# Kernel optimization log

Measured on AMD Instinct MI355X. Metric: run time of the kernel, lower is better.

## Reference

```python
import jax, jax.numpy as jnp
import numpy as np

POOL_RATIO = 0.5  # SAGPooling default ratio


def graph_conv(x, src, dst, Wr, Wn, b, num_nodes):
    # PyG GraphConv (aggr='add'): h_i = x_i Wr + (sum_{j->i} x_j) Wn + b
    agg = jax.ops.segment_sum(x[src], dst, num_segments=num_nodes)
    return x @ Wr + agg @ Wn + b


def setup_inputs() -> dict:
    key = jax.random.key(0)
    ks = jax.random.split(key, 12)
    B, M, DF = 64, 512, 128           # batch, max_num_obj, per-feature dim
    N = B * M                          # 32768 flat nodes
    E = 524288                         # avg degree 16
    D_IN, D_OUT, L, C = 256, 256, 3, 11
    s_in = 1.0 / np.sqrt(D_IN)
    f0 = jax.random.normal(ks[0], (B, M, DF), jnp.float32)
    f1 = jax.random.normal(ks[1], (B, M, DF), jnp.float32)
    collated_edge_index = jax.random.randint(ks[2], (2, E), 0, N, dtype=jnp.int32)
    Wr = jax.random.normal(ks[3], (L, D_IN, D_OUT), jnp.float32) * s_in
    Wn = jax.random.normal(ks[4], (L, D_IN, D_OUT), jnp.float32) * s_in
    b = jax.random.normal(ks[5], (L, D_OUT), jnp.float32) * 0.01
    Wpr = jax.random.normal(ks[6], (D_OUT, 1), jnp.float32) * s_in
    Wpn = jax.random.normal(ks[7], (D_OUT, 1), jnp.float32) * s_in
    bp = jax.random.normal(ks[8], (1,), jnp.float32) * 0.01
    Wc = jax.random.normal(ks[9], (D_OUT, C), jnp.float32) * s_in
    bc = jax.random.normal(ks[10], (C,), jnp.float32) * 0.01
    return {"f0": f0, "f1": f1, "collated_edge_index": collated_edge_index,
            "Wr": Wr, "Wn": Wn, "b": b, "Wpr": Wpr, "Wpn": Wpn, "bp": bp,
            "Wc": Wc, "bc": bc}


def reference(f0, f1, collated_edge_index, Wr, Wn, b, Wpr, Wpn, bp, Wc, bc):
    # concat node features then flatten batch: [B, M, 2*DF] -> [N, D_IN]
    x = jnp.concatenate([f0, f1], axis=2)
    x = x.reshape(-1, x.shape[-1])
    N = x.shape[0]
    src, dst = collated_edge_index[0], collated_edge_index[1]
    for i in range(Wr.shape[0]):  # stacked GNN blocks + ReLU
        x = jax.nn.relu(graph_conv(x, src, dst, Wr[i], Wn[i], b[i], N))
    # SAGPooling: GraphConv attention score; source's batch tensor is constant
    # so top-k runs over all N nodes as one segment (ratio 0.5)
    score = graph_conv(x, src, dst, Wpr, Wpn, bp, N)[:, 0]
    k = int(np.ceil(POOL_RATIO * N))
    top_scores, perm = jax.lax.top_k(score, k)
    xp = x[perm] * jnp.tanh(top_scores)[:, None]   # [k, D_OUT]
    xp = jax.nn.relu(xp)
    logits = xp @ Wc + bc                          # [k, 11]
    return logits
```

## Files before the change

### kernel.cpp

```cpp
#include <hip/hip_runtime.h>
#include <hip/hip_bf16.h>
#include <math.h>
#include <stdint.h>


__global__ __launch_bounds__(256) void concat_kernel(const float* __restrict__ f0,
                                                     const float* __restrict__ f1,
                                                     float* __restrict__ x,
                                                     int N) {
    int gid = blockIdx.x * blockDim.x + threadIdx.x;
    int total = N * 64;
    if (gid >= total) return;
    int n = gid >> 6;
    int q = gid & 63;
    float4 v;
    if (q < 32) v = *(const float4*)(f0 + (size_t)n * 128 + q * 4);
    else        v = *(const float4*)(f1 + (size_t)n * 128 + (q - 32) * 4);
    *(float4*)(x + (size_t)n * 256 + q * 4) = v;
}

__global__ __launch_bounds__(256) void count_kernel(const int* __restrict__ dst,
                                                    int* __restrict__ counts, int E) {
    int e = blockIdx.x * blockDim.x + threadIdx.x;
    if (e < E) atomicAdd(&counts[dst[e]], 1);
}

__global__ __launch_bounds__(1024) void scan_kernel(int* __restrict__ counts,
                                                    int* __restrict__ offs,
                                                    int N, int E) {
    __shared__ int s[1024];
    int t = threadIdx.x;
    int base = t * 32;
    int local[32];
    int sum = 0;
    #pragma unroll
    for (int j = 0; j < 32; ++j) { local[j] = counts[base + j]; sum += local[j]; }
    s[t] = sum;
    __syncthreads();
    for (int off = 1; off < 1024; off <<= 1) {
        int other = (t >= off) ? s[t - off] : 0;
        __syncthreads();
        s[t] += other;
        __syncthreads();
    }
    int run = s[t] - sum;
    #pragma unroll
    for (int j = 0; j < 32; ++j) {
        offs[base + j] = run;
        run += local[j];
        counts[base + j] = 0;
    }
    if (t == 1023) offs[N] = E;
}

__global__ __launch_bounds__(256) void fill_kernel(const int* __restrict__ dst,
                                                   const int* __restrict__ offs,
                                                   int* __restrict__ cursor,
                                                   int* __restrict__ csr, int E) {
    int e = blockIdx.x * blockDim.x + threadIdx.x;
    if (e >= E) return;
    int d = dst[e];
    int pos = offs[d] + atomicAdd(&cursor[d], 1);
    csr[pos] = e;
}

__global__ __launch_bounds__(256) void bsort_kernel(int* __restrict__ csr,
                                                    const int* __restrict__ offs,
                                                    const int* __restrict__ src,
                                                    int N) {
    int i = blockIdx.x * blockDim.x + threadIdx.x;
    if (i >= N) return;
    int beg = offs[i], end = offs[i + 1];
    for (int a = beg + 1; a < end; ++a) {
        int v = csr[a];
        int b = a - 1;
        while (b >= beg && csr[b] > v) { csr[b + 1] = csr[b]; --b; }
        csr[b + 1] = v;
    }
    for (int p = beg; p < end; ++p) csr[p] = src[csr[p]];
}

__global__ __launch_bounds__(256) void segsum_kernel(const float* __restrict__ X,
                                                     const int* __restrict__ csr,
                                                     const int* __restrict__ offs,
                                                     float* __restrict__ AGG, int N) {
    int w = threadIdx.x >> 6;
    int lane = threadIdx.x & 63;
    int n = blockIdx.x * 4 + w;
    if (n >= N) return;
    int beg = offs[n], end = offs[n + 1];
    float4 acc = make_float4(0.f, 0.f, 0.f, 0.f);
    for (int p = beg; p < end; ++p) {
        int s = csr[p];
        float4 v = *(const float4*)(X + (size_t)s * 256 + lane * 4);
        acc.x += v.x; acc.y += v.y; acc.z += v.z; acc.w += v.w;
    }
    *(float4*)(AGG + (size_t)n * 256 + lane * 4) = acc;
}

#define GBM 128
#define GBN 128
#define GBK 32

#define GEMM_LOAD_STAGE(kt)                                                          \
    {                                                                                \
        const int kb = (kt) * GBK;                                                   \
        const float* Asrc = (kb < 256) ? X : G;                                      \
        const float* Wsrc = (kb < 256) ? W1 : W2;                                    \
        const int kloc = kb & 255;                                                   \
        a_st0 = *(const float4*)(Asrc + (size_t)(rowBase + ar) * 256 + kloc + ak);   \
        a_st1 = *(const float4*)(Asrc + (size_t)(rowBase + ar + 64) * 256 + kloc + ak); \
        a_st2 = *(const float4*)(Asrc + (size_t)(rowBase + ar) * 256 + kloc + 16 + ak); \
        a_st3 = *(const float4*)(Asrc + (size_t)(rowBase + ar + 64) * 256 + kloc + 16 + ak); \
        w_st0 = *(const float4*)(Wsrc + (size_t)(kloc + wk) * 256 + colBase + wc);   \
        w_st1 = *(const float4*)(Wsrc + (size_t)(kloc + wk + 8) * 256 + colBase + wc); \
        w_st2 = *(const float4*)(Wsrc + (size_t)(kloc + wk + 16) * 256 + colBase + wc); \
        w_st3 = *(const float4*)(Wsrc + (size_t)(kloc + wk + 24) * 256 + colBase + wc); \
    }

__global__ __launch_bounds__(256) void gemm_two_kernel(const float* __restrict__ X,
                                                       const float* __restrict__ G,
                                                       const float* __restrict__ W1,
                                                       const float* __restrict__ W2,
                                                       const float* __restrict__ bias,
                                                       float* __restrict__ Y) {
    __shared__ float As[GBK][GBM + 4];
    __shared__ float Ws[GBK][GBN + 4];
    const int tid = threadIdx.x;
    const int tcol = tid & 15;
    const int trow = tid >> 4;
    const int rowBase = blockIdx.y * GBM;
    const int colBase = blockIdx.x * GBN;

    const int ar = tid >> 2;
    const int ak = (tid & 3) * 4;
    const int wk = tid >> 5;
    const int wc = (tid & 31) * 4;

    float4 a_st0, a_st1, a_st2, a_st3, w_st0, w_st1, w_st2, w_st3;

    float acc[4][4][4];
    #pragma unroll
    for (int q = 0; q < 4; ++q)
        #pragma unroll
        for (int i = 0; i < 4; ++i)
            #pragma unroll
            for (int j = 0; j < 4; ++j) acc[q][i][j] = 0.f;

    GEMM_LOAD_STAGE(0);

    for (int kt = 0; kt < 512 / GBK; ++kt) {
        __syncthreads();
        #pragma unroll
        for (int j = 0; j < 4; ++j) {
            As[ak + j][ar]           = ((const float*)&a_st0)[j];
            As[ak + j][ar + 64]      = ((const float*)&a_st1)[j];
            As[16 + ak + j][ar]      = ((const float*)&a_st2)[j];
            As[16 + ak + j][ar + 64] = ((const float*)&a_st3)[j];
        }
        *(float4*)&Ws[wk][wc]      = w_st0;
        *(float4*)&Ws[wk + 8][wc]  = w_st1;
        *(float4*)&Ws[wk + 16][wc] = w_st2;
        *(float4*)&Ws[wk + 24][wc] = w_st3;
        __syncthreads();
        if (kt < 512 / GBK - 1) GEMM_LOAD_STAGE(kt + 1);
        #pragma unroll
        for (int kk = 0; kk < GBK; ++kk) {
            float a0[4], a1[4], w0[4], w1[4];
            *(float4*)a0 = *(const float4*)&As[kk][trow * 4];
            *(float4*)a1 = *(const float4*)&As[kk][64 + trow * 4];
            *(float4*)w0 = *(const float4*)&Ws[kk][tcol * 4];
            *(float4*)w1 = *(const float4*)&Ws[kk][64 + tcol * 4];
            #pragma unroll
            for (int i = 0; i < 4; ++i)
                #pragma unroll
                for (int j = 0; j < 4; ++j) {
                    acc[0][i][j] = fmaf(a0[i], w0[j], acc[0][i][j]);
                    acc[1][i][j] = fmaf(a0[i], w1[j], acc[1][i][j]);
                    acc[2][i][j] = fmaf(a1[i], w0[j], acc[2][i][j]);
                    acc[3][i][j] = fmaf(a1[i], w1[j], acc[3][i][j]);
                }
        }
    }
    #pragma unroll
    for (int h = 0; h < 2; ++h) {
        #pragma unroll
        for (int i = 0; i < 4; ++i) {
            const int row = rowBase + h * 64 + trow * 4 + i;
            #pragma unroll
            for (int g = 0; g < 2; ++g) {
                const int colb = colBase + g * 64 + tcol * 4;
                float o[4];
                #pragma unroll
                for (int j = 0; j < 4; ++j)
                    o[j] = fmaxf(acc[h * 2 + g][i][j] + bias[colb + j], 0.f);
                *(float4*)(Y + (size_t)row * 256 + colb) = *(const float4*)&o[0];
            }
        }
    }
}

__global__ __launch_bounds__(256) void dot_kernel(const float* __restrict__ X3,
                                                  const float* __restrict__ Wpr,
                                                  const float* __restrict__ Wpn,
                                                  double* __restrict__ yr,
                                                  double* __restrict__ yn, int N) {
    int w = threadIdx.x >> 6;
    int lane = threadIdx.x & 63;
    int n = blockIdx.x * 4 + w;
    if (n >= N) return;
    float4 xv = *(const float4*)(X3 + (size_t)n * 256 + lane * 4);
    float4 wr = *(const float4*)(Wpr + lane * 4);
    float4 wn = *(const float4*)(Wpn + lane * 4);
    double dr = (double)xv.x * wr.x + (double)xv.y * wr.y +
                (double)xv.z * wr.z + (double)xv.w * wr.w;
    double dn = (double)xv.x * wn.x + (double)xv.y * wn.y +
                (double)xv.z * wn.z + (double)xv.w * wn.w;
    #pragma unroll
    for (int o = 32; o > 0; o >>= 1) {
        dr += __shfl_down(dr, o, 64);
        dn += __shfl_down(dn, o, 64);
    }
    if (lane == 0) { yr[n] = dr; yn[n] = dn; }
}

__global__ __launch_bounds__(256) void score_gather_kernel(
        const double* __restrict__ yr, const double* __restrict__ yn,
        const int* __restrict__ csr, const int* __restrict__ offs,
        const float* __restrict__ bp,
        double* __restrict__ sc, unsigned long long* __restrict__ keys, int N) {
    int n = blockIdx.x * blockDim.x + threadIdx.x;
    if (n >= N) return;
    double s = yr[n] + (double)bp[0];
    int beg = offs[n], end = offs[n + 1];
    for (int p = beg; p < end; ++p) s += yn[csr[p]];
    sc[n] = s;
    long long sb = __double_as_longlong(s);
    keys[n] = (sb < 0) ? ~(unsigned long long)sb
                       : ((unsigned long long)sb | 0x8000000000000000ULL);
}

#define RTI 1024
#define RTJ 512
__global__ __launch_bounds__(256) void rank_count_kernel(
        const unsigned long long* __restrict__ keys,
        int* __restrict__ rankcnt, int N) {
    __shared__ __align__(16) unsigned long long sk[RTJ];
    const int tid = threadIdx.x;
    const int ibase = blockIdx.y * RTI;
    const int jbase = blockIdx.x * RTJ;

    unsigned long long ki[4];
    #pragma unroll
    for (int r = 0; r < 4; ++r) ki[r] = keys[ibase + r * 256 + tid];
    for (int t = tid; t < RTJ; t += 256) sk[t] = keys[jbase + t];
    __syncthreads();

    int cnt[4] = {0, 0, 0, 0};
    if (jbase + RTJ <= ibase) {
        for (int u = 0; u < RTJ; u += 8) {
            ulonglong2 p0 = *(const ulonglong2*)&sk[u];
            ulonglong2 p1 = *(const ulonglong2*)&sk[u + 2];
            ulonglong2 p2 = *(const ulonglong2*)&sk[u + 4];
            ulonglong2 p3 = *(const ulonglong2*)&sk[u + 6];
            #pragma unroll
            for (int r = 0; r < 4; ++r) {
                cnt[r] += (int)(p0.x >= ki[r]) + (int)(p0.y >= ki[r])
                        + (int)(p1.x >= ki[r]) + (int)(p1.y >= ki[r])
                        + (int)(p2.x >= ki[r]) + (int)(p2.y >= ki[r])
                        + (int)(p3.x >= ki[r]) + (int)(p3.y >= ki[r]);
            }
        }
    } else if (jbase >= ibase + RTI) {
        for (int u = 0; u < RTJ; u += 8) {
            ulonglong2 p0 = *(const ulonglong2*)&sk[u];
            ulonglong2 p1 = *(const ulonglong2*)&sk[u + 2];
            ulonglong2 p2 = *(const ulonglong2*)&sk[u + 4];
            ulonglong2 p3 = *(const ulonglong2*)&sk[u + 6];
            #pragma unroll
            for (int r = 0; r < 4; ++r) {
                cnt[r] += (int)(p0.x > ki[r]) + (int)(p0.y > ki[r])
                        + (int)(p1.x > ki[r]) + (int)(p1.y > ki[r])
                        + (int)(p2.x > ki[r]) + (int)(p2.y > ki[r])
                        + (int)(p3.x > ki[r]) + (int)(p3.y > ki[r]);
            }
        }
    } else {
        int thr[4];
        #pragma unroll
        for (int r = 0; r < 4; ++r) thr[r] = ibase + r * 256 + tid - jbase;
        for (int u = 0; u < RTJ; ++u) {
            unsigned long long kj = sk[u];
            #pragma unroll
            for (int r = 0; r < 4; ++r)
                cnt[r] += (kj > ki[r]) || (kj == ki[r] && u < thr[r]);
        }
    }
    #pragma unroll
    for (int r = 0; r < 4; ++r)
        atomicAdd(&rankcnt[ibase + r * 256 + tid], cnt[r]);
}

__global__ __launch_bounds__(256) void rank_scatter_kernel(
        const int* __restrict__ rankcnt,
        const double* __restrict__ sc,
        int* __restrict__ perm,
        double* __restrict__ topd, int N, int K) {
    int i = blockIdx.x * blockDim.x + threadIdx.x;
    if (i >= N) return;
    int rank = rankcnt[i];
    if (rank < K) { perm[rank] = i; topd[rank] = sc[i]; }
}

__global__ __launch_bounds__(256) void out_kernel(const float* __restrict__ X3,
                                                  const int* __restrict__ perm,
                                                  const double* __restrict__ topd,
                                                  const float* __restrict__ Wc,
                                                  const float* __restrict__ bc,
                                                  float* __restrict__ out, int K) {
    int w = threadIdx.x >> 6;
    int lane = threadIdx.x & 63;
    int r = blockIdx.x * 4 + w;
    if (r >= K) return;
    int p = perm[r];
    double t = tanh(topd[r]);
    float4 xv = *(const float4*)(X3 + (size_t)p * 256 + lane * 4);
    double xp[4];
    xp[0] = (double)xv.x * t; xp[1] = (double)xv.y * t;
    xp[2] = (double)xv.z * t; xp[3] = (double)xv.w * t;
    #pragma unroll
    for (int j = 0; j < 4; ++j) xp[j] = xp[j] > 0.0 ? xp[j] : 0.0;
    double acc[11];
    #pragma unroll
    for (int c = 0; c < 11; ++c) acc[c] = 0.0;
    #pragma unroll
    for (int j = 0; j < 4; ++j) {
        const float* wrow = Wc + (size_t)(lane * 4 + j) * 11;
        #pragma unroll
        for (int c = 0; c < 11; ++c) acc[c] += xp[j] * (double)wrow[c];
    }
    #pragma unroll
    for (int c = 0; c < 11; ++c) {
        double v = acc[c];
        #pragma unroll
        for (int o = 32; o > 0; o >>= 1) v += __shfl_down(v, o, 64);
        if (lane == 0) out[(size_t)r * 11 + c] = (float)(v + (double)bc[c]);
    }
}

extern "C" void kernel_launch(void* const* d_in, const int* in_sizes, int n_in,
                              void* d_out, int out_size, void* d_ws, size_t ws_size,
                              hipStream_t stream) {
    const float* f0  = (const float*)d_in[0];
    const float* f1  = (const float*)d_in[1];
    const int*   ei  = (const int*)d_in[2];
    const float* Wr  = (const float*)d_in[3];
    const float* Wn  = (const float*)d_in[4];
    const float* b   = (const float*)d_in[5];
    const float* Wpr = (const float*)d_in[6];
    const float* Wpn = (const float*)d_in[7];
    const float* bp  = (const float*)d_in[8];
    const float* Wc  = (const float*)d_in[9];
    const float* bc  = (const float*)d_in[10];
    float* out = (float*)d_out;

    const int N = in_sizes[0] / 128;
    const int E = in_sizes[2] / 2;
    const int K = (N + 1) / 2;
    const int L = in_sizes[5] / 256;

    const int* src = ei;
    const int* dst = ei + E;

    char* p = (char*)d_ws;
    auto take = [&](size_t bytes) {
        char* r = p;
        p += (bytes + 255) & ~(size_t)255;
        return r;
    };
    float*  xA      = (float*)take((size_t)N * 256 * 4);
    float*  xB      = (float*)take((size_t)N * 256 * 4);
    float*  agg     = (float*)take((size_t)N * 256 * 4);
    int*    counts  = (int*)take((size_t)N * 4);
    int*    offs    = (int*)take((size_t)(N + 1) * 4);
    int*    csr     = (int*)take((size_t)E * 4);
    double* sc      = (double*)take((size_t)N * 8);
    unsigned long long* keys = (unsigned long long*)take((size_t)N * 8);
    int*    rankcnt = (int*)take((size_t)N * 4);
    double* topd    = (double*)take((size_t)K * 8);
    int*    perm    = (int*)take((size_t)K * 4);
    double* yrv     = (double*)take((size_t)N * 8);
    double* ynv     = (double*)take((size_t)N * 8);
    (void)ws_size;

    hipMemsetAsync(counts, 0, (size_t)N * 4, stream);
    hipMemsetAsync(rankcnt, 0, (size_t)N * 4, stream);

    concat_kernel<<<(N * 64 + 255) / 256, 256, 0, stream>>>(f0, f1, xA, N);
    count_kernel<<<(E + 255) / 256, 256, 0, stream>>>(dst, counts, E);
    scan_kernel<<<1, 1024, 0, stream>>>(counts, offs, N, E);
    fill_kernel<<<(E + 255) / 256, 256, 0, stream>>>(dst, offs, counts, csr, E);
    bsort_kernel<<<(N + 255) / 256, 256, 0, stream>>>(csr, offs, src, N);

    float* xcur = xA;
    float* xnext = xB;
    for (int i = 0; i < L; ++i) {
        segsum_kernel<<<N / 4, 256, 0, stream>>>(xcur, csr, offs, agg, N);
        gemm_two_kernel<<<dim3(256 / GBN, N / GBM), 256, 0, stream>>>(
            xcur, agg, Wr + (size_t)i * 65536, Wn + (size_t)i * 65536,
            b + (size_t)i * 256, xnext);
        float* tmp = xcur; xcur = xnext; xnext = tmp;
    }
    dot_kernel<<<N / 4, 256, 0, stream>>>(xcur, Wpr, Wpn, yrv, ynv, N);
    score_gather_kernel<<<N / 256, 256, 0, stream>>>(yrv, ynv, csr, offs, bp, sc, keys, N);
    rank_count_kernel<<<dim3(N / RTJ, N / RTI), 256, 0, stream>>>(keys, rankcnt, N);
    rank_scatter_kernel<<<(N + 255) / 256, 256, 0, stream>>>(rankcnt, sc, perm, topd, N, K);
    out_kernel<<<K / 4, 256, 0, stream>>>(xcur, perm, topd, Wc, bc, out, K);
}
```

Before: 813.5 us.

## Split two-operand GEMM into K-split partial products plus combine-ReLU pass

```diff
diff --git a/kernel.cpp b/kernel.cpp
--- a/kernel.cpp
+++ b/kernel.cpp
@@ -101,6 +101,122 @@
 #define GBM 128
 #define GBN 128
 #define GBK 32
+
+#define GSPLIT_LOAD(kt)                                                              \
+    {                                                                                \
+        const int kloc = (kt) * GBK;                                                 \
+        a_st0 = *(const float4*)(A + (size_t)(rowBase + ar) * 256 + kloc + ak);      \
+        a_st1 = *(const float4*)(A + (size_t)(rowBase + ar + 64) * 256 + kloc + ak); \
+        a_st2 = *(const float4*)(A + (size_t)(rowBase + ar) * 256 + kloc + 16 + ak); \
+        a_st3 = *(const float4*)(A + (size_t)(rowBase + ar + 64) * 256 + kloc + 16 + ak); \
+        w_st0 = *(const float4*)(W + (size_t)(kloc + wk) * 256 + colBase + wc);      \
+        w_st1 = *(const float4*)(W + (size_t)(kloc + wk + 8) * 256 + colBase + wc);  \
+        w_st2 = *(const float4*)(W + (size_t)(kloc + wk + 16) * 256 + colBase + wc); \
+        w_st3 = *(const float4*)(W + (size_t)(kloc + wk + 24) * 256 + colBase + wc); \
+    }
+
+__global__ __launch_bounds__(256, 4) void gemm_split_kernel(
+        const float* __restrict__ X, const float* __restrict__ G,
+        const float* __restrict__ W1, const float* __restrict__ W2,
+        const float* __restrict__ bias,
+        float* __restrict__ P1, float* __restrict__ P2) {
+    __shared__ float As[GBK][GBM + 4];
+    __shared__ float Ws[GBK][GBN + 4];
+    const int tid = threadIdx.x;
+    const int tcol = tid & 15;
+    const int trow = tid >> 4;
+    const int rowBase = blockIdx.y * GBM;
+    const int colBase = blockIdx.x * GBN;
+    const int z = blockIdx.z;
+    const float* __restrict__ A = z ? G : X;
+    const float* __restrict__ W = z ? W2 : W1;
+    float* __restrict__ P = z ? P2 : P1;
+
+    const int ar = tid >> 2;
+    const int ak = (tid & 3) * 4;
+    const int wk = tid >> 5;
+    const int wc = (tid & 31) * 4;
+
+    float4 a_st0, a_st1, a_st2, a_st3, w_st0, w_st1, w_st2, w_st3;
+
+    float acc[4][4][4];
+    #pragma unroll
+    for (int q = 0; q < 4; ++q)
+        #pragma unroll
+        for (int i = 0; i < 4; ++i)
+            #pragma unroll
+            for (int j = 0; j < 4; ++j) acc[q][i][j] = 0.f;
+
+    GSPLIT_LOAD(0);
+
+    for (int kt = 0; kt < 256 / GBK; ++kt) {
+        __syncthreads();
+        #pragma unroll
+        for (int j = 0; j < 4; ++j) {
+            As[ak + j][ar]           = ((const float*)&a_st0)[j];
+            As[ak + j][ar + 64]      = ((const float*)&a_st1)[j];
+            As[16 + ak + j][ar]      = ((const float*)&a_st2)[j];
+            As[16 + ak + j][ar + 64] = ((const float*)&a_st3)[j];
+        }
+        *(float4*)&Ws[wk][wc]      = w_st0;
+        *(float4*)&Ws[wk + 8][wc]  = w_st1;
+        *(float4*)&Ws[wk + 16][wc] = w_st2;
+        *(float4*)&Ws[wk + 24][wc] = w_st3;
+        __syncthreads();
+        if (kt < 256 / GBK - 1) GSPLIT_LOAD(kt + 1);
+        #pragma unroll
+        for (int kk = 0; kk < GBK; ++kk) {
+            float a0[4], a1[4], w0[4], w1[4];
+            *(float4*)a0 = *(const float4*)&As[kk][trow * 4];
+            *(float4*)a1 = *(const float4*)&As[kk][64 + trow * 4];
+            *(float4*)w0 = *(const float4*)&Ws[kk][tcol * 4];
+            *(float4*)w1 = *(const float4*)&Ws[kk][64 + tcol * 4];
+            #pragma unroll
+            for (int i = 0; i < 4; ++i)
+                #pragma unroll
+                for (int j = 0; j < 4; ++j) {
+                    acc[0][i][j] = fmaf(a0[i], w0[j], acc[0][i][j]);
+                    acc[1][i][j] = fmaf(a0[i], w1[j], acc[1][i][j]);
+                    acc[2][i][j] = fmaf(a1[i], w0[j], acc[2][i][j]);
+                    acc[3][i][j] = fmaf(a1[i], w1[j], acc[3][i][j]);
+                }
+        }
+    }
+    #pragma unroll
+    for (int h = 0; h < 2; ++h) {
+        #pragma unroll
+        for (int i = 0; i < 4; ++i) {
+            const int row = rowBase + h * 64 + trow * 4 + i;
+            #pragma unroll
+            for (int g = 0; g < 2; ++g) {
+                const int colb = colBase + g * 64 + tcol * 4;
+                float o[4];
+                #pragma unroll
+                for (int j = 0; j < 4; ++j) {
+                    float v = acc[h * 2 + g][i][j];
+                    if (z == 0) v += bias[colb + j];
+                    o[j] = v;
+                }
+                *(float4*)(P + (size_t)row * 256 + colb) = *(const float4*)&o[0];
+            }
+        }
+    }
+}
+
+__global__ __launch_bounds__(256) void combine_relu_kernel(
+        const float* __restrict__ P1, const float* __restrict__ P2,
+        float* __restrict__ Y, int total4) {
+    int gid = blockIdx.x * 256 + threadIdx.x;
+    if (gid >= total4) return;
+    float4 a = ((const float4*)P1)[gid];
+    float4 b = ((const float4*)P2)[gid];
+    float4 o;
+    o.x = fmaxf(a.x + b.x, 0.f);
+    o.y = fmaxf(a.y + b.y, 0.f);
+    o.z = fmaxf(a.z + b.z, 0.f);
+    o.w = fmaxf(a.w + b.w, 0.f);
+    ((float4*)Y)[gid] = o;
+}
 
 #define GEMM_LOAD_STAGE(kt)                                                          \
     {                                                                                \
@@ -391,7 +507,8 @@
     int*    perm    = (int*)take((size_t)K * 4);
     double* yrv     = (double*)take((size_t)N * 8);
     double* ynv     = (double*)take((size_t)N * 8);
-    (void)ws_size;
+    float*  P2buf   = (float*)take((size_t)N * 256 * 4);
+    const bool use_split = (size_t)(p - (char*)d_ws) <= ws_size;
 
     hipMemsetAsync(counts, 0, (size_t)N * 4, stream);
     hipMemsetAsync(rankcnt, 0, (size_t)N * 4, stream);
@@ -406,9 +523,17 @@
     float* xnext = xB;
     for (int i = 0; i < L; ++i) {
         segsum_kernel<<<N / 4, 256, 0, stream>>>(xcur, csr, offs, agg, N);
-        gemm_two_kernel<<<dim3(256 / GBN, N / GBM), 256, 0, stream>>>(
-            xcur, agg, Wr + (size_t)i * 65536, Wn + (size_t)i * 65536,
-            b + (size_t)i * 256, xnext);
+        if (use_split) {
+            gemm_split_kernel<<<dim3(256 / GBN, N / GBM, 2), 256, 0, stream>>>(
+                xcur, agg, Wr + (size_t)i * 65536, Wn + (size_t)i * 65536,
+                b + (size_t)i * 256, xnext, P2buf);
+            combine_relu_kernel<<<(N * 64 + 255) / 256, 256, 0, stream>>>(
+                xnext, P2buf, xnext, N * 64);
+        } else {
+            gemm_two_kernel<<<dim3(256 / GBN, N / GBM), 256, 0, stream>>>(
+                xcur, agg, Wr + (size_t)i * 65536, Wn + (size_t)i * 65536,
+                b + (size_t)i * 256, xnext);
+        }
         float* tmp = xcur; xcur = xnext; xnext = tmp;
     }
     dot_kernel<<<N / 4, 256, 0, stream>>>(xcur, Wpr, Wpn, yrv, ynv, N);
```

Result: slower. 1.335 ms (+64.1%).

## Split GEMM into two K-halves across grid z and add combine-ReLU kernel

Applied to the files above, without the earlier changes.

```diff
diff --git a/kernel.cpp b/kernel.cpp
--- a/kernel.cpp
+++ b/kernel.cpp
@@ -100,104 +100,119 @@
 
 #define GBM 128
 #define GBN 128
-#define GBK 32
-
-#define GEMM_LOAD_STAGE(kt)                                                          \
-    {                                                                                \
-        const int kb = (kt) * GBK;                                                   \
-        const float* Asrc = (kb < 256) ? X : G;                                      \
-        const float* Wsrc = (kb < 256) ? W1 : W2;                                    \
-        const int kloc = kb & 255;                                                   \
-        a_st0 = *(const float4*)(Asrc + (size_t)(rowBase + ar) * 256 + kloc + ak);   \
-        a_st1 = *(const float4*)(Asrc + (size_t)(rowBase + ar + 64) * 256 + kloc + ak); \
-        a_st2 = *(const float4*)(Asrc + (size_t)(rowBase + ar) * 256 + kloc + 16 + ak); \
-        a_st3 = *(const float4*)(Asrc + (size_t)(rowBase + ar + 64) * 256 + kloc + 16 + ak); \
-        w_st0 = *(const float4*)(Wsrc + (size_t)(kloc + wk) * 256 + colBase + wc);   \
-        w_st1 = *(const float4*)(Wsrc + (size_t)(kloc + wk + 8) * 256 + colBase + wc); \
-        w_st2 = *(const float4*)(Wsrc + (size_t)(kloc + wk + 16) * 256 + colBase + wc); \
-        w_st3 = *(const float4*)(Wsrc + (size_t)(kloc + wk + 24) * 256 + colBase + wc); \
-    }
-
-__global__ __launch_bounds__(256) void gemm_two_kernel(const float* __restrict__ X,
-                                                       const float* __restrict__ G,
-                                                       const float* __restrict__ W1,
-                                                       const float* __restrict__ W2,
-                                                       const float* __restrict__ bias,
-                                                       float* __restrict__ Y) {
+#define GBK 16
+
+#define GSPLIT_LOAD(kt)                                                          \
+    {                                                                             \
+        const int kloc = (kt) * GBK;                                              \
+        const float* Abase = A + (size_t)(rowBase + tid) * 256 + kloc;            \
+        a_st0 = *(const float4*)(Abase + 0);                                      \
+        a_st1 = *(const float4*)(Abase + 4);                                      \
+        a_st2 = *(const float4*)(Abase + 8);                                      \
+        a_st3 = *(const float4*)(Abase + 12);                                     \
+        const float* Wbase = W + (size_t)(kloc + wk) * 256 + colBase + wc;        \
+        w_st0 = *(const float4*)(Wbase + 0);                                      \
+        w_st1 = *(const float4*)(Wbase + 4);                                      \
+        w_st2 = *(const float4*)(Wbase + 8);                                      \
+        w_st3 = *(const float4*)(Wbase + 12);                                     \
+    }
+
+__global__ __launch_bounds__(128) void gemm_split_kernel(
+        const float* __restrict__ X, const float* __restrict__ G,
+        const float* __restrict__ W1, const float* __restrict__ W2,
+        const float* __restrict__ bias,
+        float* __restrict__ P1, float* __restrict__ P2) {
     __shared__ float As[GBK][GBM + 4];
     __shared__ float Ws[GBK][GBN + 4];
     const int tid = threadIdx.x;
+    const int trow = tid >> 4;
     const int tcol = tid & 15;
-    const int trow = tid >> 4;
     const int rowBase = blockIdx.y * GBM;
     const int colBase = blockIdx.x * GBN;
-
-    const int ar = tid >> 2;
-    const int ak = (tid & 3) * 4;
-    const int wk = tid >> 5;
-    const int wc = (tid & 31) * 4;
+    const int z = blockIdx.z;
+    const float* __restrict__ A = z ? G : X;
+    const float* __restrict__ W = z ? W2 : W1;
+    float* __restrict__ P = z ? P2 : P1;
+
+    const int wk = tid >> 3;
+    const int wc = (tid & 7) * 16;
 
     float4 a_st0, a_st1, a_st2, a_st3, w_st0, w_st1, w_st2, w_st3;
 
-    float acc[4][4][4];
-    #pragma unroll
-    for (int q = 0; q < 4; ++q)
-        #pragma unroll
-        for (int i = 0; i < 4; ++i)
-            #pragma unroll
-            for (int j = 0; j < 4; ++j) acc[q][i][j] = 0.f;
-
-    GEMM_LOAD_STAGE(0);
-
-    for (int kt = 0; kt < 512 / GBK; ++kt) {
+    float acc[2][16][4];
+    #pragma unroll
+    for (int h = 0; h < 2; ++h)
+        #pragma unroll
+        for (int i = 0; i < 16; ++i)
+            #pragma unroll
+            for (int j = 0; j < 4; ++j) acc[h][i][j] = 0.f;
+
+    GSPLIT_LOAD(0);
+
+    for (int kt = 0; kt < 256 / GBK; ++kt) {
         __syncthreads();
         #pragma unroll
         for (int j = 0; j < 4; ++j) {
-            As[ak + j][ar]           = ((const float*)&a_st0)[j];
-            As[ak + j][ar + 64]      = ((const float*)&a_st1)[j];
-            As[16 + ak + j][ar]      = ((const float*)&a_st2)[j];
-            As[16 + ak + j][ar + 64] = ((const float*)&a_st3)[j];
+            As[j][tid]      = ((const float*)&a_st0)[j];
+            As[4 + j][tid]  = ((const float*)&a_st1)[j];
+            As[8 + j][tid]  = ((const float*)&a_st2)[j];
+            As[12 + j][tid] = ((const float*)&a_st3)[j];
         }
         *(float4*)&Ws[wk][wc]      = w_st0;
-        *(float4*)&Ws[wk + 8][wc]  = w_st1;
-        *(float4*)&Ws[wk + 16][wc] = w_st2;
-        *(float4*)&Ws[wk + 24][wc] = w_st3;
+        *(float4*)&Ws[wk][wc + 4]  = w_st1;
+        *(float4*)&Ws[wk][wc + 8]  = w_st2;
+        *(float4*)&Ws[wk][wc + 12] = w_st3;
         __syncthreads();
-        if (kt < 512 / GBK - 1) GEMM_LOAD_STAGE(kt + 1);
+        if (kt < 256 / GBK - 1) GSPLIT_LOAD(kt + 1);
         #pragma unroll
         for (int kk = 0; kk < GBK; ++kk) {
-            float a0[4], a1[4], w0[4], w1[4];
-            *(float4*)a0 = *(const float4*)&As[kk][trow * 4];
-            *(float4*)a1 = *(const float4*)&As[kk][64 + trow * 4];
-            *(float4*)w0 = *(const float4*)&Ws[kk][tcol * 4];
-            *(float4*)w1 = *(const float4*)&Ws[kk][64 + tcol * 4];
-            #pragma unroll
-            for (int i = 0; i < 4; ++i)
+            float a[16], w[8];
+            *(float4*)&a[0]  = *(const float4*)&As[kk][trow * 16];
+            *(float4*)&a[4]  = *(const float4*)&As[kk][trow * 16 + 4];
+            *(float4*)&a[8]  = *(const float4*)&As[kk][trow * 16 + 8];
+            *(float4*)&a[12] = *(const float4*)&As[kk][trow * 16 + 12];
+            *(float4*)&w[0]  = *(const float4*)&Ws[kk][tcol * 4];
+            *(float4*)&w[4]  = *(const float4*)&Ws[kk][64 + tcol * 4];
+            #pragma unroll
+            for (int i = 0; i < 16; ++i)
                 #pragma unroll
                 for (int j = 0; j < 4; ++j) {
-                    acc[0][i][j] = fmaf(a0[i], w0[j], acc[0][i][j]);
-                    acc[1][i][j] = fmaf(a0[i], w1[j], acc[1][i][j]);
-                    acc[2][i][j] = fmaf(a1[i], w0[j], acc[2][i][j]);
-                    acc[3][i][j] = fmaf(a1[i], w1[j], acc[3][i][j]);
+                    acc[0][i][j] = fmaf(a[i], w[j],     acc[0][i][j]);
+                    acc[1][i][j] = fmaf(a[i], w[4 + j], acc[1][i][j]);
                 }
         }
     }
     #pragma unroll
-    for (int h = 0; h < 2; ++h) {
-        #pragma unroll
-        for (int i = 0; i < 4; ++i) {
-            const int row = rowBase + h * 64 + trow * 4 + i;
-            #pragma unroll
-            for (int g = 0; g < 2; ++g) {
-                const int colb = colBase + g * 64 + tcol * 4;
-                float o[4];
-                #pragma unroll
-                for (int j = 0; j < 4; ++j)
-                    o[j] = fmaxf(acc[h * 2 + g][i][j] + bias[colb + j], 0.f);
-                *(float4*)(Y + (size_t)row * 256 + colb) = *(const float4*)&o[0];
+    for (int i = 0; i < 16; ++i) {
+        const int row = rowBase + trow * 16 + i;
+        #pragma unroll
+        for (int h = 0; h < 2; ++h) {
+            const int colb = colBase + h * 64 + tcol * 4;
+            float o[4];
+            #pragma unroll
+            for (int j = 0; j < 4; ++j) {
+                float v = acc[h][i][j];
+                if (z == 0) v += bias[colb + j];
+                o[j] = v;
             }
-        }
-    }
+            *(float4*)(P + (size_t)row * 256 + colb) = *(const float4*)&o[0];
+        }
+    }
+}
+
+__global__ __launch_bounds__(256) void combine_relu_kernel(
+        const float* __restrict__ P1, const float* __restrict__ P2,
+        float* __restrict__ Y, int total4) {
+    int gid = blockIdx.x * 256 + threadIdx.x;
+    if (gid >= total4) return;
+    float4 a = ((const float4*)P1)[gid];
+    float4 b = ((const float4*)P2)[gid];
+    float4 o;
+    o.x = fmaxf(a.x + b.x, 0.f);
+    o.y = fmaxf(a.y + b.y, 0.f);
+    o.z = fmaxf(a.z + b.z, 0.f);
+    o.w = fmaxf(a.w + b.w, 0.f);
+    ((float4*)Y)[gid] = o;
 }
 
 __global__ __launch_bounds__(256) void dot_kernel(const float* __restrict__ X3,
@@ -391,6 +406,7 @@
     int*    perm    = (int*)take((size_t)K * 4);
     double* yrv     = (double*)take((size_t)N * 8);
     double* ynv     = (double*)take((size_t)N * 8);
+    float*  P2buf   = (float*)take((size_t)N * 256 * 4);
     (void)ws_size;
 
     hipMemsetAsync(counts, 0, (size_t)N * 4, stream);
@@ -406,9 +422,11 @@
     float* xnext = xB;
     for (int i = 0; i < L; ++i) {
         segsum_kernel<<<N / 4, 256, 0, stream>>>(xcur, csr, offs, agg, N);
-        gemm_two_kernel<<<dim3(256 / GBN, N / GBM), 256, 0, stream>>>(
+        gemm_split_kernel<<<dim3(256 / GBN, N / GBM, 2), 128, 0, stream>>>(
             xcur, agg, Wr + (size_t)i * 65536, Wn + (size_t)i * 65536,
-            b + (size_t)i * 256, xnext);
+            b + (size_t)i * 256, xnext, P2buf);
+        combine_relu_kernel<<<(N * 64 + 255) / 256, 256, 0, stream>>>(
+            xnext, P2buf, xnext, N * 64);
         float* tmp = xcur; xcur = xnext; xnext = tmp;
     }
     dot_kernel<<<N / 4, 256, 0, stream>>>(xcur, Wpr, Wpn, yrv, ynv, N);
```

New measurement: 973.7 us. 1.2x slower.
